# Kernel optimization log

Hardware: AMD Instinct MI355X
Metric: run time of the kernel (lower is better)

Reference implementation:

```python
import jax, jax.numpy as jnp
import numpy as np


def binarize(t):
    # torch.where(t > 0, +1, -1)
    return jnp.where(t > 0, jnp.float32(1.0), jnp.float32(-1.0))


def setup_inputs() -> dict:
    key = jax.random.key(0)
    k1, k2, k3 = jax.random.split(key, 3)
    N, D_IN, D_OUT = 8192, 4096, 4096
    x = jax.random.normal(k1, (N, D_IN), dtype=jnp.float32)
    weight = jax.random.normal(k2, (D_OUT, D_IN), dtype=jnp.float32) * 0.02
    bias = jax.random.normal(k3, (D_OUT,), dtype=jnp.float32) * 0.02
    return {"x": x, "weight": weight, "bias": bias}


def reference(x, weight, bias):
    # Binarize input and weight to +/-1, then standard float linear: y = bx @ bw^T + b
    bx = binarize(x)          # [N, D_in]
    bw = binarize(weight)     # [D_out, D_in]
    return jnp.einsum('ni,oi->no', bx, bw) + bias
```

## Files before the change

kernel.cpp:

```cpp
#include <hip/hip_runtime.h>
#include <stdint.h>

using i32x4 = __attribute__((ext_vector_type(4))) int;
using i32x8 = __attribute__((ext_vector_type(8))) int;
using f32x4 = __attribute__((ext_vector_type(4))) float;

#define M_ROWS 8192
#define N_COLS 4096
#define K_DIM  4096
#define KB_ROW 2048
#define BM 256
#define BN 256
#define TKB 128
#define NT (KB_ROW / TKB)
#define SC1 0x7F7F7F7F

__global__ __launch_bounds__(256) void binarize_fp4_kernel(
    const float4* __restrict__ in, unsigned* __restrict__ out, int n_out) {
  int idx = blockIdx.x * blockDim.x + threadIdx.x;
  int stride = gridDim.x * blockDim.x;
  for (int i = idx; i < n_out; i += stride) {
    float4 a = in[2 * i], b = in[2 * i + 1];
    unsigned neg =
        ((a.x > 0.f ? 0u : 1u) << 3)  | ((a.y > 0.f ? 0u : 1u) << 7)  |
        ((a.z > 0.f ? 0u : 1u) << 11) | ((a.w > 0.f ? 0u : 1u) << 15) |
        ((b.x > 0.f ? 0u : 1u) << 19) | ((b.y > 0.f ? 0u : 1u) << 23) |
        ((b.z > 0.f ? 0u : 1u) << 27) | ((b.w > 0.f ? 0u : 1u) << 31);
    out[i] = 0x22222222u | neg;
  }
}

#define GLOAD(gsrc, ldst)                                                    \
  __builtin_amdgcn_global_load_lds(                                          \
      (const __attribute__((address_space(1))) void*)(gsrc),                 \
      (__attribute__((address_space(3))) void*)(ldst), 16, 0, 0)


#define STG_A(NB, KBo, KH)                                                   \
  GLOAD(aS0 + (KBo) + (KH) * 64, As + (NB) + (KH) * 16384 + dstW);           \
  GLOAD(aS1 + (KBo) + (KH) * 64, As + (NB) + (KH) * 16384 + 8192 + dstW)

#define STG_B(NB, KBo, KH)                                                   \
  GLOAD(bS0 + (KBo) + (KH) * 64, Bs + (NB) + (KH) * 16384 + dstW);           \
  GLOAD(bS1 + (KBo) + (KH) * 64, Bs + (NB) + (KH) * 16384 + 8192 + dstW)

#define DO_PHASE(BUFOFF, KHOFF, MH, BLOAD, STAGE_STMT, PRE_CLOSE)            \
  {                                                                          \
    STAGE_STMT                                                               \
    if (BLOAD) {                                                             \
      _Pragma("unroll")                                                      \
      for (int nf = 0; nf < 4; ++nf)                                         \
        *(i32x4*)&bf8[nf] =                                                  \
            *(const i32x4*)(Bs + (BUFOFF) + (KHOFF) + bRdOff + nf * 1024);   \
    }                                                                        \
    _Pragma("unroll")                                                        \
    for (int mf = 0; mf < 4; ++mf)                                           \
      *(i32x4*)&af8[mf] = *(const i32x4*)(As + (BUFOFF) + (KHOFF) +          \
                                          aRdOff + (MH) * 4096 + mf * 1024); \
    __builtin_amdgcn_s_barrier();                                            \
    __builtin_amdgcn_s_setprio(1);                                           \
    _Pragma("unroll")                                                        \
    for (int mf = 0; mf < 4; ++mf) {                                         \
      _Pragma("unroll")                                                      \
      for (int nf = 0; nf < 4; ++nf)                                         \
        acc[(MH) * 4 + mf][nf] =                                             \
            __builtin_amdgcn_mfma_scale_f32_16x16x128_f8f6f4(                \
                af8[mf], bf8[nf], acc[(MH) * 4 + mf][nf], 4, 4, 0, SC1, 0,   \
                SC1);                                                        \
    }                                                                        \
    __builtin_amdgcn_s_setprio(0);                                           \
    PRE_CLOSE                                                                \
    __builtin_amdgcn_s_barrier();                                            \
  }

#define TILE_NORMAL(BUFOFF, NBUFOFF, KBo)                                    \
  DO_PHASE(BUFOFF, 0, 0, true, STG_A(NBUFOFF, KBo, 0);, )                    \
  DO_PHASE(BUFOFF, 0, 1, false, STG_B(NBUFOFF, KBo, 0);,                     \
           asm volatile("s_waitcnt vmcnt(4)" ::: "memory");)                 \
  DO_PHASE(BUFOFF, 16384, 0, true, STG_A(NBUFOFF, KBo, 1);, )                \
  DO_PHASE(BUFOFF, 16384, 1, false, STG_B(NBUFOFF, KBo, 1);,                 \
           asm volatile("s_waitcnt vmcnt(4)" ::: "memory");)

#define TILE_LAST(BUFOFF)                                                    \
  DO_PHASE(BUFOFF, 0, 0, true, , )                                           \
  DO_PHASE(BUFOFF, 0, 1, false, ,                                            \
           asm volatile("s_waitcnt vmcnt(0)" ::: "memory");)                 \
  DO_PHASE(BUFOFF, 16384, 0, true, , )                                       \
  DO_PHASE(BUFOFF, 16384, 1, false, , )

__global__ __launch_bounds__(512, 2) void bgemm_fp4_8ph(
    const unsigned char* __restrict__ xa, const unsigned char* __restrict__ wb,
    const float* __restrict__ bias, float* __restrict__ y) {
  __shared__ __align__(16) unsigned char As[65536];
  __shared__ __align__(16) unsigned char Bs[65536];

  const int tid  = threadIdx.x;
  const int lane = tid & 63;
  const int w8   = tid >> 6;
  const int wr   = w8 >> 2;
  const int wc   = w8 & 3;

  const int id = blockIdx.x;
  const int sw = ((id & 7) << 6) | (id >> 3);
  const int by = sw >> 4;
  const int bx = sw & 15;
  const int m0 = by * BM;
  const int n0 = bx * BN;

  const int r0  = tid >> 2;
  const int gsl = (((tid & 3) ^ ((tid >> 3) & 3)) << 4);
  const unsigned char* aS0 = xa + (size_t)(m0 + r0) * KB_ROW + gsl;
  const unsigned char* aS1 = xa + (size_t)(m0 + 128 + r0) * KB_ROW + gsl;
  const unsigned char* bS0 = wb + (size_t)(n0 + r0) * KB_ROW + gsl;
  const unsigned char* bS1 = wb + (size_t)(n0 + 128 + r0) * KB_ROW + gsl;
  const int dstW = w8 * 1024;

  const int lr  = lane & 15;
  const int kq  = lane >> 4;
  const int rsw = (kq ^ ((lr >> 1) & 3)) << 4;
  const int aRdOff = (wr * 128 + lr) * 64 + rsw;
  const int bRdOff = (wc * 64 + lr) * 64 + rsw;

  f32x4 acc[8][4];
#pragma unroll
  for (int i = 0; i < 8; ++i)
#pragma unroll
    for (int j = 0; j < 4; ++j) acc[i][j] = (f32x4){0.f, 0.f, 0.f, 0.f};

  i32x8 af8[4], bf8[4];
#pragma unroll
  for (int i = 0; i < 4; ++i) {
    af8[i] = (i32x8){0, 0, 0, 0, 0, 0, 0, 0};
    bf8[i] = (i32x8){0, 0, 0, 0, 0, 0, 0, 0};
  }

  STG_A(0, 0, 0);
  STG_B(0, 0, 0);
  STG_A(0, 0, 1);
  STG_B(0, 0, 1);
  asm volatile("s_waitcnt vmcnt(4)" ::: "memory");
  __builtin_amdgcn_s_barrier();

#pragma unroll 1
  for (int tp = 0; tp < 7; ++tp) {
    const int kb1 = tp * 256 + 128;
    const int kb2 = tp * 256 + 256;
    TILE_NORMAL(0, 32768, kb1)
    TILE_NORMAL(32768, 0, kb2)
  }
  TILE_NORMAL(0, 32768, 1920)
  TILE_LAST(32768)

  float bv[4];
#pragma unroll
  for (int nf = 0; nf < 4; ++nf) bv[nf] = bias[n0 + wc * 64 + nf * 16 + lr];
#pragma unroll
  for (int fr = 0; fr < 8; ++fr) {
#pragma unroll
    for (int j = 0; j < 4; ++j) {
      const int gr = m0 + wr * 128 + fr * 16 + kq * 4 + j;
      float* orow = y + (size_t)gr * N_COLS + n0 + wc * 64 + lr;
#pragma unroll
      for (int nf = 0; nf < 4; ++nf)
        orow[nf * 16] = acc[fr][nf][j] + bv[nf];
    }
  }
}

extern "C" void kernel_launch(void* const* d_in, const int* in_sizes, int n_in,
                              void* d_out, int out_size, void* d_ws, size_t ws_size,
                              hipStream_t stream) {
  const float* x    = (const float*)d_in[0];
  const float* wgt  = (const float*)d_in[1];
  const float* bias = (const float*)d_in[2];
  float* y = (float*)d_out;

  unsigned char* xa = (unsigned char*)d_ws;
  unsigned char* wb = xa + (size_t)M_ROWS * KB_ROW;

  binarize_fp4_kernel<<<2048, 256, 0, stream>>>(
      (const float4*)x, (unsigned*)xa, (M_ROWS * K_DIM) / 8);
  binarize_fp4_kernel<<<2048, 256, 0, stream>>>(
      (const float4*)wgt, (unsigned*)wb, (N_COLS * K_DIM) / 8);

  bgemm_fp4_8ph<<<512, 512, 0, stream>>>(xa, wb, bias, y);
}
```

Measured before the change: 131.1 us.

## Shrink GEMM tiles to 128x128 and fuse the two binarize launches

The FP4 MFMA GEMM tile drops from 256x256 to 128x128, which halves the LDS buffers and per-warp fragments, raises the occupancy target to 4 blocks per CU, and launches 2048 blocks instead of 512. The two binarize kernels are merged into one launch that covers x and weight back to back in the workspace. The smaller tiles are meant to improve load balance and occupancy across the CUs. In exchange each output now needs twice the global and LDS operand traffic, and each barrier-separated phase holds only 4 MFMAs, so load latency may be harder to hide.

```diff
diff --git a/kernel.cpp b/kernel.cpp
--- a/kernel.cpp
+++ b/kernel.cpp
@@ -9,18 +9,23 @@
 #define N_COLS 4096
 #define K_DIM  4096
 #define KB_ROW 2048
-#define BM 256
-#define BN 256
+#define BM 128
+#define BN 128
 #define TKB 128
 #define NT (KB_ROW / TKB)
 #define SC1 0x7F7F7F7F
 
-__global__ __launch_bounds__(256) void binarize_fp4_kernel(
-    const float4* __restrict__ in, unsigned* __restrict__ out, int n_out) {
-  int idx = blockIdx.x * blockDim.x + threadIdx.x;
-  int stride = gridDim.x * blockDim.x;
-  for (int i = idx; i < n_out; i += stride) {
-    float4 a = in[2 * i], b = in[2 * i + 1];
+#define XDW   ((size_t)M_ROWS * K_DIM / 8)
+#define TOTDW (((size_t)(M_ROWS + N_COLS)) * K_DIM / 8)
+__global__ __launch_bounds__(256) void binarize_fp4_fused(
+    const float4* __restrict__ x, const float4* __restrict__ w,
+    unsigned* __restrict__ out) {
+  size_t idx = (size_t)blockIdx.x * blockDim.x + threadIdx.x;
+  size_t stride = (size_t)gridDim.x * blockDim.x;
+  for (size_t i = idx; i < TOTDW; i += stride) {
+    const float4* src = (i < XDW) ? x : w;
+    size_t j = (i < XDW) ? i : (i - XDW);
+    float4 a = src[2 * j], b = src[2 * j + 1];
     unsigned neg =
         ((a.x > 0.f ? 0u : 1u) << 3)  | ((a.y > 0.f ? 0u : 1u) << 7)  |
         ((a.z > 0.f ? 0u : 1u) << 11) | ((a.w > 0.f ? 0u : 1u) << 15) |
@@ -37,35 +42,33 @@
 
 
 #define STG_A(NB, KBo, KH)                                                   \
-  GLOAD(aS0 + (KBo) + (KH) * 64, As + (NB) + (KH) * 16384 + dstW);           \
-  GLOAD(aS1 + (KBo) + (KH) * 64, As + (NB) + (KH) * 16384 + 8192 + dstW)
+  GLOAD(aS0 + (KBo) + (KH) * 64, As + (NB) + (KH) * 8192 + dstW)
 
 #define STG_B(NB, KBo, KH)                                                   \
-  GLOAD(bS0 + (KBo) + (KH) * 64, Bs + (NB) + (KH) * 16384 + dstW);           \
-  GLOAD(bS1 + (KBo) + (KH) * 64, Bs + (NB) + (KH) * 16384 + 8192 + dstW)
+  GLOAD(bS0 + (KBo) + (KH) * 64, Bs + (NB) + (KH) * 8192 + dstW)
 
 #define DO_PHASE(BUFOFF, KHOFF, MH, BLOAD, STAGE_STMT, PRE_CLOSE)            \
   {                                                                          \
     STAGE_STMT                                                               \
     if (BLOAD) {                                                             \
       _Pragma("unroll")                                                      \
-      for (int nf = 0; nf < 4; ++nf)                                         \
+      for (int nf = 0; nf < 2; ++nf)                                         \
         *(i32x4*)&bf8[nf] =                                                  \
             *(const i32x4*)(Bs + (BUFOFF) + (KHOFF) + bRdOff + nf * 1024);   \
     }                                                                        \
     _Pragma("unroll")                                                        \
-    for (int mf = 0; mf < 4; ++mf)                                           \
+    for (int mf = 0; mf < 2; ++mf)                                           \
       *(i32x4*)&af8[mf] = *(const i32x4*)(As + (BUFOFF) + (KHOFF) +          \
-                                          aRdOff + (MH) * 4096 + mf * 1024); \
+                                          aRdOff + (MH) * 2048 + mf * 1024); \
     __builtin_amdgcn_s_barrier();                                            \
     __builtin_amdgcn_s_setprio(1);                                           \
     _Pragma("unroll")                                                        \
-    for (int mf = 0; mf < 4; ++mf) {                                         \
+    for (int mf = 0; mf < 2; ++mf) {                                         \
       _Pragma("unroll")                                                      \
-      for (int nf = 0; nf < 4; ++nf)                                         \
-        acc[(MH) * 4 + mf][nf] =                                             \
+      for (int nf = 0; nf < 2; ++nf)                                         \
+        acc[(MH) * 2 + mf][nf] =                                             \
             __builtin_amdgcn_mfma_scale_f32_16x16x128_f8f6f4(                \
-                af8[mf], bf8[nf], acc[(MH) * 4 + mf][nf], 4, 4, 0, SC1, 0,   \
+                af8[mf], bf8[nf], acc[(MH) * 2 + mf][nf], 4, 4, 0, SC1, 0,   \
                 SC1);                                                        \
     }                                                                        \
     __builtin_amdgcn_s_setprio(0);                                           \
@@ -76,23 +79,23 @@
 #define TILE_NORMAL(BUFOFF, NBUFOFF, KBo)                                    \
   DO_PHASE(BUFOFF, 0, 0, true, STG_A(NBUFOFF, KBo, 0);, )                    \
   DO_PHASE(BUFOFF, 0, 1, false, STG_B(NBUFOFF, KBo, 0);,                     \
-           asm volatile("s_waitcnt vmcnt(4)" ::: "memory");)                 \
-  DO_PHASE(BUFOFF, 16384, 0, true, STG_A(NBUFOFF, KBo, 1);, )                \
-  DO_PHASE(BUFOFF, 16384, 1, false, STG_B(NBUFOFF, KBo, 1);,                 \
-           asm volatile("s_waitcnt vmcnt(4)" ::: "memory");)
+           asm volatile("s_waitcnt vmcnt(2)" ::: "memory");)                 \
+  DO_PHASE(BUFOFF, 8192, 0, true, STG_A(NBUFOFF, KBo, 1);, )                 \
+  DO_PHASE(BUFOFF, 8192, 1, false, STG_B(NBUFOFF, KBo, 1);,                  \
+           asm volatile("s_waitcnt vmcnt(2)" ::: "memory");)
 
 #define TILE_LAST(BUFOFF)                                                    \
   DO_PHASE(BUFOFF, 0, 0, true, , )                                           \
   DO_PHASE(BUFOFF, 0, 1, false, ,                                            \
            asm volatile("s_waitcnt vmcnt(0)" ::: "memory");)                 \
-  DO_PHASE(BUFOFF, 16384, 0, true, , )                                       \
-  DO_PHASE(BUFOFF, 16384, 1, false, , )
+  DO_PHASE(BUFOFF, 8192, 0, true, , )                                        \
+  DO_PHASE(BUFOFF, 8192, 1, false, , )
 
-__global__ __launch_bounds__(512, 2) void bgemm_fp4_8ph(
+__global__ __launch_bounds__(512, 4) void bgemm_fp4_128(
     const unsigned char* __restrict__ xa, const unsigned char* __restrict__ wb,
     const float* __restrict__ bias, float* __restrict__ y) {
-  __shared__ __align__(16) unsigned char As[65536];
-  __shared__ __align__(16) unsigned char Bs[65536];
+  __shared__ __align__(16) unsigned char As[32768];
+  __shared__ __align__(16) unsigned char Bs[32768];
 
   const int tid  = threadIdx.x;
   const int lane = tid & 63;
@@ -101,35 +104,33 @@
   const int wc   = w8 & 3;
 
   const int id = blockIdx.x;
-  const int sw = ((id & 7) << 6) | (id >> 3);
-  const int by = sw >> 4;
-  const int bx = sw & 15;
+  const int sw = ((id & 7) << 8) | (id >> 3);
+  const int by = sw >> 5;
+  const int bx = sw & 31;
   const int m0 = by * BM;
   const int n0 = bx * BN;
 
   const int r0  = tid >> 2;
   const int gsl = (((tid & 3) ^ ((tid >> 3) & 3)) << 4);
   const unsigned char* aS0 = xa + (size_t)(m0 + r0) * KB_ROW + gsl;
-  const unsigned char* aS1 = xa + (size_t)(m0 + 128 + r0) * KB_ROW + gsl;
   const unsigned char* bS0 = wb + (size_t)(n0 + r0) * KB_ROW + gsl;
-  const unsigned char* bS1 = wb + (size_t)(n0 + 128 + r0) * KB_ROW + gsl;
   const int dstW = w8 * 1024;
 
   const int lr  = lane & 15;
   const int kq  = lane >> 4;
   const int rsw = (kq ^ ((lr >> 1) & 3)) << 4;
-  const int aRdOff = (wr * 128 + lr) * 64 + rsw;
-  const int bRdOff = (wc * 64 + lr) * 64 + rsw;
+  const int aRdOff = (wr * 64 + lr) * 64 + rsw;
+  const int bRdOff = (wc * 32 + lr) * 64 + rsw;
 
-  f32x4 acc[8][4];
+  f32x4 acc[4][2];
 #pragma unroll
-  for (int i = 0; i < 8; ++i)
+  for (int i = 0; i < 4; ++i)
 #pragma unroll
-    for (int j = 0; j < 4; ++j) acc[i][j] = (f32x4){0.f, 0.f, 0.f, 0.f};
+    for (int j = 0; j < 2; ++j) acc[i][j] = (f32x4){0.f, 0.f, 0.f, 0.f};
 
-  i32x8 af8[4], bf8[4];
+  i32x8 af8[2], bf8[2];
 #pragma unroll
-  for (int i = 0; i < 4; ++i) {
+  for (int i = 0; i < 2; ++i) {
     af8[i] = (i32x8){0, 0, 0, 0, 0, 0, 0, 0};
     bf8[i] = (i32x8){0, 0, 0, 0, 0, 0, 0, 0};
   }
@@ -138,30 +139,30 @@
   STG_B(0, 0, 0);
   STG_A(0, 0, 1);
   STG_B(0, 0, 1);
-  asm volatile("s_waitcnt vmcnt(4)" ::: "memory");
+  asm volatile("s_waitcnt vmcnt(2)" ::: "memory");
   __builtin_amdgcn_s_barrier();
 
 #pragma unroll 1
   for (int tp = 0; tp < 7; ++tp) {
     const int kb1 = tp * 256 + 128;
     const int kb2 = tp * 256 + 256;
-    TILE_NORMAL(0, 32768, kb1)
-    TILE_NORMAL(32768, 0, kb2)
+    TILE_NORMAL(0, 16384, kb1)
+    TILE_NORMAL(16384, 0, kb2)
   }
-  TILE_NORMAL(0, 32768, 1920)
-  TILE_LAST(32768)
+  TILE_NORMAL(0, 16384, 1920)
+  TILE_LAST(16384)
 
-  float bv[4];
+  float bv[2];
 #pragma unroll
-  for (int nf = 0; nf < 4; ++nf) bv[nf] = bias[n0 + wc * 64 + nf * 16 + lr];
+  for (int nf = 0; nf < 2; ++nf) bv[nf] = bias[n0 + wc * 32 + nf * 16 + lr];
 #pragma unroll
-  for (int fr = 0; fr < 8; ++fr) {
+  for (int fr = 0; fr < 4; ++fr) {
 #pragma unroll
     for (int j = 0; j < 4; ++j) {
-      const int gr = m0 + wr * 128 + fr * 16 + kq * 4 + j;
-      float* orow = y + (size_t)gr * N_COLS + n0 + wc * 64 + lr;
+      const int gr = m0 + wr * 64 + fr * 16 + kq * 4 + j;
+      float* orow = y + (size_t)gr * N_COLS + n0 + wc * 32 + lr;
 #pragma unroll
-      for (int nf = 0; nf < 4; ++nf)
+      for (int nf = 0; nf < 2; ++nf)
         orow[nf * 16] = acc[fr][nf][j] + bv[nf];
     }
   }
@@ -178,10 +179,9 @@
   unsigned char* xa = (unsigned char*)d_ws;
   unsigned char* wb = xa + (size_t)M_ROWS * KB_ROW;
 
-  binarize_fp4_kernel<<<2048, 256, 0, stream>>>(
-      (const float4*)x, (unsigned*)xa, (M_ROWS * K_DIM) / 8);
-  binarize_fp4_kernel<<<2048, 256, 0, stream>>>(
-      (const float4*)wgt, (unsigned*)wb, (N_COLS * K_DIM) / 8);
+  binarize_fp4_fused<<<2048, 256, 0, stream>>>(
+      (const float4*)x, (const float4*)wgt, (unsigned*)xa);
 
-  bgemm_fp4_8ph<<<512, 512, 0, stream>>>(xa, wb, bias, y);
+  dim3 grid((M_ROWS / BM) * (N_COLS / BN));
+  bgemm_fp4_128<<<grid, 512, 0, stream>>>(xa, wb, bias, y);
 }
```

After: 147.7 us. +12.7%, slower.

## Fuse binarize launches and restructure GEMM to two barriers per tile

Applied to the files above, without the earlier changes.

Merges the two binarize kernels into one launch over x and w, with each thread packing 16 floats into two words. The GEMM K-tile drops from four phases with two barriers each to two phases with one barrier each. Each phase loads all B fragments and streams the A fragments through a two-register ring, so fewer A registers are held. This cuts launch overhead and barrier stalls, but LDS reads of A are now interleaved with the MFMAs and may expose LDS latency.

```diff
diff --git a/kernel.cpp b/kernel.cpp
--- a/kernel.cpp
+++ b/kernel.cpp
@@ -15,18 +15,32 @@
 #define NT (KB_ROW / TKB)
 #define SC1 0x7F7F7F7F
 
-__global__ __launch_bounds__(256) void binarize_fp4_kernel(
-    const float4* __restrict__ in, unsigned* __restrict__ out, int n_out) {
-  int idx = blockIdx.x * blockDim.x + threadIdx.x;
-  int stride = gridDim.x * blockDim.x;
-  for (int i = idx; i < n_out; i += stride) {
-    float4 a = in[2 * i], b = in[2 * i + 1];
-    unsigned neg =
-        ((a.x > 0.f ? 0u : 1u) << 3)  | ((a.y > 0.f ? 0u : 1u) << 7)  |
-        ((a.z > 0.f ? 0u : 1u) << 11) | ((a.w > 0.f ? 0u : 1u) << 15) |
-        ((b.x > 0.f ? 0u : 1u) << 19) | ((b.y > 0.f ? 0u : 1u) << 23) |
-        ((b.z > 0.f ? 0u : 1u) << 27) | ((b.w > 0.f ? 0u : 1u) << 31);
-    out[i] = 0x22222222u | neg;
+#define XDW   ((size_t)M_ROWS * K_DIM / 8)
+#define TOTDW (((size_t)(M_ROWS + N_COLS)) * K_DIM / 8)
+
+__device__ __forceinline__ unsigned pack8(float4 a, float4 b) {
+  unsigned neg =
+      ((a.x > 0.f ? 0u : 1u) << 3)  | ((a.y > 0.f ? 0u : 1u) << 7)  |
+      ((a.z > 0.f ? 0u : 1u) << 11) | ((a.w > 0.f ? 0u : 1u) << 15) |
+      ((b.x > 0.f ? 0u : 1u) << 19) | ((b.y > 0.f ? 0u : 1u) << 23) |
+      ((b.z > 0.f ? 0u : 1u) << 27) | ((b.w > 0.f ? 0u : 1u) << 31);
+  return 0x22222222u | neg;
+}
+
+__global__ __launch_bounds__(256) void binarize_fp4_fused(
+    const float4* __restrict__ x, const float4* __restrict__ w,
+    unsigned* __restrict__ out) {
+  size_t u = (size_t)blockIdx.x * blockDim.x + threadIdx.x;
+  size_t stride = (size_t)gridDim.x * blockDim.x;
+  for (; u < TOTDW / 2; u += stride) {
+    size_t d = u * 2;
+    const float4* s;
+    size_t j;
+    if (d < XDW) { s = x; j = d * 2; }
+    else         { s = w; j = (d - XDW) * 2; }
+    float4 f0 = s[j], f1 = s[j + 1], f2 = s[j + 2], f3 = s[j + 3];
+    out[d]     = pack8(f0, f1);
+    out[d + 1] = pack8(f2, f3);
   }
 }
 
@@ -44,51 +58,44 @@
   GLOAD(bS0 + (KBo) + (KH) * 64, Bs + (NB) + (KH) * 16384 + dstW);           \
   GLOAD(bS1 + (KBo) + (KH) * 64, Bs + (NB) + (KH) * 16384 + 8192 + dstW)
 
-#define DO_PHASE(BUFOFF, KHOFF, MH, BLOAD, STAGE_STMT, PRE_CLOSE)            \
+#define VM4BAR                                                               \
+  asm volatile("s_waitcnt vmcnt(4)" ::: "memory");                           \
+  __builtin_amdgcn_s_barrier();
+
+#define VM0BAR                                                               \
+  asm volatile("s_waitcnt vmcnt(0)" ::: "memory");                           \
+  __builtin_amdgcn_s_barrier();
+
+#define DO_PHASE(BUFOFF, KHOFF, STAGE_STMT, CLOSE_STMT)                      \
   {                                                                          \
     STAGE_STMT                                                               \
-    if (BLOAD) {                                                             \
+    _Pragma("unroll")                                                        \
+    for (int nf = 0; nf < 4; ++nf)                                           \
+      *(i32x4*)&bf8[nf] =                                                    \
+          *(const i32x4*)(Bs + (BUFOFF) + (KHOFF) + bRdOff + nf * 1024);     \
+    __builtin_amdgcn_s_setprio(1);                                           \
+    _Pragma("unroll")                                                        \
+    for (int fr = 0; fr < 8; ++fr) {                                         \
+      *(i32x4*)&af8[fr & 1] =                                                \
+          *(const i32x4*)(As + (BUFOFF) + (KHOFF) + aRdOff + fr * 1024);     \
       _Pragma("unroll")                                                      \
       for (int nf = 0; nf < 4; ++nf)                                         \
-        *(i32x4*)&bf8[nf] =                                                  \
-            *(const i32x4*)(Bs + (BUFOFF) + (KHOFF) + bRdOff + nf * 1024);   \
-    }                                                                        \
-    _Pragma("unroll")                                                        \
-    for (int mf = 0; mf < 4; ++mf)                                           \
-      *(i32x4*)&af8[mf] = *(const i32x4*)(As + (BUFOFF) + (KHOFF) +          \
-                                          aRdOff + (MH) * 4096 + mf * 1024); \
-    __builtin_amdgcn_s_barrier();                                            \
-    __builtin_amdgcn_s_setprio(1);                                           \
-    _Pragma("unroll")                                                        \
-    for (int mf = 0; mf < 4; ++mf) {                                         \
-      _Pragma("unroll")                                                      \
-      for (int nf = 0; nf < 4; ++nf)                                         \
-        acc[(MH) * 4 + mf][nf] =                                             \
-            __builtin_amdgcn_mfma_scale_f32_16x16x128_f8f6f4(                \
-                af8[mf], bf8[nf], acc[(MH) * 4 + mf][nf], 4, 4, 0, SC1, 0,   \
-                SC1);                                                        \
+        acc[fr][nf] = __builtin_amdgcn_mfma_scale_f32_16x16x128_f8f6f4(      \
+            af8[fr & 1], bf8[nf], acc[fr][nf], 4, 4, 0, SC1, 0, SC1);        \
     }                                                                        \
     __builtin_amdgcn_s_setprio(0);                                           \
-    PRE_CLOSE                                                                \
-    __builtin_amdgcn_s_barrier();                                            \
+    CLOSE_STMT                                                               \
   }
 
-#define TILE_NORMAL(BUFOFF, NBUFOFF, KBo)                                    \
-  DO_PHASE(BUFOFF, 0, 0, true, STG_A(NBUFOFF, KBo, 0);, )                    \
-  DO_PHASE(BUFOFF, 0, 1, false, STG_B(NBUFOFF, KBo, 0);,                     \
-           asm volatile("s_waitcnt vmcnt(4)" ::: "memory");)                 \
-  DO_PHASE(BUFOFF, 16384, 0, true, STG_A(NBUFOFF, KBo, 1);, )                \
-  DO_PHASE(BUFOFF, 16384, 1, false, STG_B(NBUFOFF, KBo, 1);,                 \
-           asm volatile("s_waitcnt vmcnt(4)" ::: "memory");)
+#define TILE(BUF, NBUF, KBo)                                                 \
+  DO_PHASE(BUF, 0,     STG_A(NBUF, KBo, 0); STG_B(NBUF, KBo, 0);, VM4BAR)    \
+  DO_PHASE(BUF, 16384, STG_A(NBUF, KBo, 1); STG_B(NBUF, KBo, 1);, VM4BAR)
 
-#define TILE_LAST(BUFOFF)                                                    \
-  DO_PHASE(BUFOFF, 0, 0, true, , )                                           \
-  DO_PHASE(BUFOFF, 0, 1, false, ,                                            \
-           asm volatile("s_waitcnt vmcnt(0)" ::: "memory");)                 \
-  DO_PHASE(BUFOFF, 16384, 0, true, , )                                       \
-  DO_PHASE(BUFOFF, 16384, 1, false, , )
+#define TILE_LAST(BUF)                                                       \
+  DO_PHASE(BUF, 0, , VM0BAR)                                                 \
+  DO_PHASE(BUF, 16384, , )
 
-__global__ __launch_bounds__(512, 2) void bgemm_fp4_8ph(
+__global__ __launch_bounds__(512, 2) void bgemm_fp4_2bar(
     const unsigned char* __restrict__ xa, const unsigned char* __restrict__ wb,
     const float* __restrict__ bias, float* __restrict__ y) {
   __shared__ __align__(16) unsigned char As[65536];
@@ -127,12 +134,11 @@
 #pragma unroll
     for (int j = 0; j < 4; ++j) acc[i][j] = (f32x4){0.f, 0.f, 0.f, 0.f};
 
-  i32x8 af8[4], bf8[4];
+  i32x8 af8[2], bf8[4];
 #pragma unroll
-  for (int i = 0; i < 4; ++i) {
-    af8[i] = (i32x8){0, 0, 0, 0, 0, 0, 0, 0};
-    bf8[i] = (i32x8){0, 0, 0, 0, 0, 0, 0, 0};
-  }
+  for (int i = 0; i < 2; ++i) af8[i] = (i32x8){0, 0, 0, 0, 0, 0, 0, 0};
+#pragma unroll
+  for (int i = 0; i < 4; ++i) bf8[i] = (i32x8){0, 0, 0, 0, 0, 0, 0, 0};
 
   STG_A(0, 0, 0);
   STG_B(0, 0, 0);
@@ -145,10 +151,10 @@
   for (int tp = 0; tp < 7; ++tp) {
     const int kb1 = tp * 256 + 128;
     const int kb2 = tp * 256 + 256;
-    TILE_NORMAL(0, 32768, kb1)
-    TILE_NORMAL(32768, 0, kb2)
+    TILE(0, 32768, kb1)
+    TILE(32768, 0, kb2)
   }
-  TILE_NORMAL(0, 32768, 1920)
+  TILE(0, 32768, 1920)
   TILE_LAST(32768)
 
   float bv[4];
@@ -178,10 +184,8 @@
   unsigned char* xa = (unsigned char*)d_ws;
   unsigned char* wb = xa + (size_t)M_ROWS * KB_ROW;
 
-  binarize_fp4_kernel<<<2048, 256, 0, stream>>>(
-      (const float4*)x, (unsigned*)xa, (M_ROWS * K_DIM) / 8);
-  binarize_fp4_kernel<<<2048, 256, 0, stream>>>(
-      (const float4*)wgt, (unsigned*)wb, (N_COLS * K_DIM) / 8);
+  binarize_fp4_fused<<<4096, 256, 0, stream>>>(
+      (const float4*)x, (const float4*)wgt, (unsigned*)xa);
 
-  bgemm_fp4_8ph<<<512, 512, 0, stream>>>(xa, wb, bias, y);
+  bgemm_fp4_2bar<<<512, 512, 0, stream>>>(xa, wb, bias, y);
 }
```

Result: no change. 131.5 us (+0.3%).
